# Kernel optimization log

Hardware: AMD Instinct MI355X
Metric: run time of the kernel (lower is better)

Reference implementation:

```python
import jax, jax.numpy as jnp
import numpy as np

N_NODES = 100000


def setup_inputs() -> dict:
    key = jax.random.key(0)
    k1, k2, k3, k4, k5 = jax.random.split(key, 5)
    dim_in, dim_out = 128, 128
    x = jax.random.normal(k1, (N_NODES, dim_in), dtype=jnp.float32)
    edge_index = jax.random.randint(k2, (2, 1600000), 0, N_NODES, dtype=jnp.int64)
    # PyG SAGEConv params: lin_l (neighbor path, with bias), lin_r (root path, no bias)
    s = 1.0 / np.sqrt(dim_in)
    W_l = jax.random.uniform(k3, (dim_in, dim_out), jnp.float32, -s, s)
    b_l = jax.random.uniform(k4, (dim_out,), jnp.float32, -s, s)
    W_r = jax.random.uniform(k5, (dim_in, dim_out), jnp.float32, -s, s)
    return {"x": x, "edge_index": edge_index, "W_l": W_l, "b_l": b_l, "W_r": W_r}


def reference(x, edge_index, W_l, b_l, W_r):
    src, dst = edge_index[0], edge_index[1]
    # mean aggregation of source features onto target nodes
    gathered = x[src]                                   # [E, d_in]
    summed = jax.ops.segment_sum(gathered, dst, num_segments=N_NODES)
    ones = jnp.ones((edge_index.shape[1],), dtype=x.dtype)
    count = jax.ops.segment_sum(ones, dst, num_segments=N_NODES)
    agg = summed / jnp.maximum(count, 1.0)[:, None]     # [N, d_in]
    # out = lin_l(agg) + lin_r(x)
    return agg @ W_l + b_l + x @ W_r
```

## Files before the change

kernel.cpp:

```cpp
#include <hip/hip_runtime.h>

#define N_NODES 100000
#define DIM 128
#define NE 1600000
#define NTILES (N_NODES / 8)
#define GEMM_BLOCKS 2048
#define CHUNK 512
#define NCHUNK ((N_NODES + CHUNK - 1) / CHUNK)

#define WT_BLOCKS 128
#define NCOARSE 391
#define CPAD 16
#define CCAP 4608
#define CB_BLOCKS 512
#define EPA (NE / CB_BLOCKS)
#define BCAP 640
#define NFINE 3125
#define BK_CAP 1024

typedef unsigned short u16;
typedef __attribute__((ext_vector_type(8))) short bf16x8;
typedef __attribute__((ext_vector_type(4))) float f32x4;

__device__ __forceinline__ float bf2f(u16 h) {
  return __uint_as_float(((unsigned int)h) << 16);
}
__device__ __forceinline__ u16 f2bf(float f) {
  unsigned int u = __float_as_uint(f);
  unsigned int lsb = (u >> 16) & 1u;
  u += 0x7fffu + lsb;
  return (u16)(u >> 16);
}


__global__ __launch_bounds__(256) void prep_k(const float* __restrict__ x,
                                              const float* __restrict__ Wl,
                                              const float* __restrict__ Wr,
                                              u16* __restrict__ Ax,
                                              u16* __restrict__ Wt,
                                              int* __restrict__ curC) {
  const int blk = blockIdx.x;
  if (blk < WT_BLOCKS) {
    int idx = blk * 256 + threadIdx.x;
    if (idx < NCOARSE * CPAD) curC[idx] = 0;
    int n = idx >> 8;
    int k = idx & 255;
    float v = (k < 128) ? Wr[(size_t)k * DIM + n] : Wl[(size_t)(k - 128) * DIM + n];
    Wt[(size_t)n * 256 + k] = f2bf(v);
    return;
  }
  int t = (blk - WT_BLOCKS) * 256 + threadIdx.x;
  int row = t >> 5;
  int c = (t & 31) * 4;
  float4 v = *(const float4*)(x + (size_t)row * DIM + c);
  ushort4 o;
  o.x = f2bf(v.x); o.y = f2bf(v.y); o.z = f2bf(v.z); o.w = f2bf(v.w);
  *(ushort4*)(Ax + (size_t)row * DIM + c) = o;
}

__global__ __launch_bounds__(512) void coarse_bin_k(const int* __restrict__ ei,
                                                    int* __restrict__ curC,
                                                    int* __restrict__ binnedC) {
  __shared__ u16 keyS[EPA];
  __shared__ int recS[EPA];
  __shared__ u16 key2[EPA];
  __shared__ int rec2[EPA];
  __shared__ int hist[NCOARSE];
  __shared__ int off[NCOARSE];
  __shared__ int lcur[NCOARSE];
  __shared__ int gbase[NCOARSE];
  __shared__ int scanb[512];
  const int tid = threadIdx.x;
  const int e0 = blockIdx.x * EPA;

  for (int i = tid; i < NCOARSE; i += 512) hist[i] = 0;
  __syncthreads();
  for (int i = tid; i < EPA; i += 512) {
    int src = ei[e0 + i];
    int dst = ei[NE + e0 + i];
    keyS[i] = (u16)(dst >> 8);
    recS[i] = ((dst & 255) << 17) | src;
    atomicAdd(&hist[dst >> 8], 1);
  }
  __syncthreads();
  int v = (tid < NCOARSE) ? hist[tid] : 0;
  scanb[tid] = v;
  __syncthreads();
  for (int o = 1; o < 512; o <<= 1) {
    int add = (tid >= o) ? scanb[tid - o] : 0;
    __syncthreads();
    scanb[tid] += add;
    __syncthreads();
  }
  if (tid < NCOARSE) {
    int ex = scanb[tid] - v;
    off[tid] = ex;
    lcur[tid] = ex;
    gbase[tid] = v ? atomicAdd(&curC[tid * CPAD], v) : 0;
  }
  __syncthreads();
  for (int i = tid; i < EPA; i += 512) {
    int k = keyS[i];
    int p = atomicAdd(&lcur[k], 1);
    rec2[p] = recS[i];
    key2[p] = (u16)k;
  }
  __syncthreads();
  for (int i = tid; i < EPA; i += 512) {
    int k = key2[i];
    int gp = gbase[k] + (i - off[k]);
    if (gp < CCAP) binnedC[(size_t)k * CCAP + gp] = rec2[i];
  }
}

__global__ __launch_bounds__(256) void fine_bin_k(const int* __restrict__ curC,
                                                  const int* __restrict__ binnedC,
                                                  int* __restrict__ binned,
                                                  int* __restrict__ bcnt) {
  __shared__ int recS[CCAP];
  __shared__ int rec2[CCAP];
  __shared__ int hist[8];
  __shared__ int off[8];
  __shared__ int lcur[8];
  const int c = blockIdx.x;
  const int tid = threadIdx.x;
  int cnt = curC[c * CPAD];
  if (cnt > CCAP) cnt = CCAP;

  if (tid < 8) hist[tid] = 0;
  __syncthreads();
  for (int i = tid; i < cnt; i += 256) {
    int r = binnedC[(size_t)c * CCAP + i];
    recS[i] = r;
    atomicAdd(&hist[r >> 22], 1);
  }
  __syncthreads();
  if (tid < 8) {
    int vv = hist[tid];
    bcnt[c * 8 + tid] = vv > BCAP ? BCAP : vv;
  }
  if (tid == 0) {
    int a = 0;
#pragma unroll
    for (int k = 0; k < 8; ++k) { off[k] = a; lcur[k] = a; a += hist[k]; }
  }
  __syncthreads();
  for (int i = tid; i < cnt; i += 256) {
    int r = recS[i];
    int p = atomicAdd(&lcur[r >> 22], 1);
    rec2[p] = r;
  }
  __syncthreads();
  for (int i = tid; i < cnt; i += 256) {
    int r = rec2[i];
    int k = r >> 22;
    int sl = i - off[k];
    if (sl < BCAP)
      binned[(size_t)(c * 8 + k) * BCAP + sl] = r & 0x3FFFFF;
  }
}

__global__ __launch_bounds__(256) void aggGemm_k(const int* __restrict__ bcnt,
                                                 const int* __restrict__ binned,
                                                 const u16* __restrict__ Ax,
                                                 const u16* __restrict__ Wt,
                                                 const float* __restrict__ bias,
                                                 float* __restrict__ out) {
  __shared__ int recS[BK_CAP];
  __shared__ int srcS[BK_CAP];
  __shared__ u16 aggS[32][136];
  __shared__ int hist[32];
  __shared__ int off[32];
  __shared__ int cur[32];
  const int b = blockIdx.x;
  const size_t lo = (size_t)b * BCAP;
  int cnt = bcnt[b];
  if (cnt > BK_CAP) cnt = BK_CAP;

  if (threadIdx.x < 32) hist[threadIdx.x] = 0;
  __syncthreads();
  for (int i = threadIdx.x; i < cnt; i += 256) {
    int rec = __builtin_nontemporal_load(&binned[lo + i]);
    recS[i] = rec;
    atomicAdd(&hist[rec >> 17], 1);
  }
  __syncthreads();
  if (threadIdx.x < 32) off[threadIdx.x] = hist[threadIdx.x];
  __syncthreads();
  for (int st = 1; st < 32; st <<= 1) {
    int add = 0;
    if (threadIdx.x < 32 && threadIdx.x >= st) add = off[threadIdx.x - st];
    __syncthreads();
    if (threadIdx.x < 32) off[threadIdx.x] += add;
    __syncthreads();
  }
  if (threadIdx.x < 32) cur[threadIdx.x] = off[threadIdx.x] - hist[threadIdx.x];
  __syncthreads();
  for (int i = threadIdx.x; i < cnt; i += 256) {
    int rec = recS[i];
    int l = atomicAdd(&cur[rec >> 17], 1);
    srcS[l] = (rec & 0x1FFFF) << 7;
  }
  __syncthreads();

  const int wave = threadIdx.x >> 6;
  const int lane = threadIdx.x & 63;
  const int half = lane >> 5;
  const int l5 = lane & 31;
  for (int ln = wave; ln < 32; ln += 4) {
    int d = hist[ln];
    int e1 = off[ln];
    int j = e1 - d;
    float a0 = 0.f, a1 = 0.f, a2 = 0.f, a3 = 0.f;
    for (; j + 4 <= e1; j += 4) {
      int sA = srcS[j + half];
      int sB = srcS[j + 2 + half];
      uint2 uA = *(const uint2*)(Ax + (size_t)(sA + l5 * 4));
      uint2 uB = *(const uint2*)(Ax + (size_t)(sB + l5 * 4));
      a0 += bf2f((u16)uA.x) + bf2f((u16)uB.x);
      a1 += bf2f((u16)(uA.x >> 16)) + bf2f((u16)(uB.x >> 16));
      a2 += bf2f((u16)uA.y) + bf2f((u16)uB.y);
      a3 += bf2f((u16)(uA.y >> 16)) + bf2f((u16)(uB.y >> 16));
    }
    if (j + 2 <= e1) {
      int sA = srcS[j + half];
      uint2 uA = *(const uint2*)(Ax + (size_t)(sA + l5 * 4));
      a0 += bf2f((u16)uA.x);
      a1 += bf2f((u16)(uA.x >> 16));
      a2 += bf2f((u16)uA.y);
      a3 += bf2f((u16)(uA.y >> 16));
      j += 2;
    }
    if (j < e1 && half == 0) {
      int sA = srcS[j];
      uint2 uA = *(const uint2*)(Ax + (size_t)(sA + l5 * 4));
      a0 += bf2f((u16)uA.x);
      a1 += bf2f((u16)(uA.x >> 16));
      a2 += bf2f((u16)uA.y);
      a3 += bf2f((u16)(uA.y >> 16));
    }
    a0 += __shfl_xor(a0, 32);
    a1 += __shfl_xor(a1, 32);
    a2 += __shfl_xor(a2, 32);
    a3 += __shfl_xor(a3, 32);
    if (half == 0) {
      float scale = 1.0f / fmaxf((float)d, 1.0f);
      uint2 pp;
      pp.x = (unsigned)f2bf(a0 * scale) | ((unsigned)f2bf(a1 * scale) << 16);
      pp.y = (unsigned)f2bf(a2 * scale) | ((unsigned)f2bf(a3 * scale) << 16);
      *(uint2*)&((unsigned*)aggS)[ln * 68 + l5 * 2] = pp;
    }
  }
  __syncthreads();

  const int m = lane & 15;
  const int q = lane >> 4;
  const int n0 = wave * 32;
  const float b0 = bias[n0 + m];
  const float b1 = bias[n0 + 16 + m];
  const u16* bp0 = Wt + (size_t)(n0 + m) * 256 + q * 8;
  const u16* bp1 = Wt + (size_t)(n0 + 16 + m) * 256 + q * 8;

#pragma clang loop unroll(disable)
  for (int t = 0; t < 2; ++t) {
    const int row = b * 32 + t * 16 + m;
    f32x4 acc0 = {0.f, 0.f, 0.f, 0.f};
    f32x4 acc1 = {0.f, 0.f, 0.f, 0.f};
    {
      const u16* apx = Ax + (size_t)row * DIM + q * 8;
      bf16x8 A0 = *(const bf16x8*)(apx + 0 * 32);
      bf16x8 A1 = *(const bf16x8*)(apx + 1 * 32);
      bf16x8 A2 = *(const bf16x8*)(apx + 2 * 32);
      bf16x8 A3 = *(const bf16x8*)(apx + 3 * 32);
      acc0 = __builtin_amdgcn_mfma_f32_16x16x32_bf16(A0, *(const bf16x8*)(bp0 + 0 * 32), acc0, 0, 0, 0);
      acc1 = __builtin_amdgcn_mfma_f32_16x16x32_bf16(A0, *(const bf16x8*)(bp1 + 0 * 32), acc1, 0, 0, 0);
      acc0 = __builtin_amdgcn_mfma_f32_16x16x32_bf16(A1, *(const bf16x8*)(bp0 + 1 * 32), acc0, 0, 0, 0);
      acc1 = __builtin_amdgcn_mfma_f32_16x16x32_bf16(A1, *(const bf16x8*)(bp1 + 1 * 32), acc1, 0, 0, 0);
      acc0 = __builtin_amdgcn_mfma_f32_16x16x32_bf16(A2, *(const bf16x8*)(bp0 + 2 * 32), acc0, 0, 0, 0);
      acc1 = __builtin_amdgcn_mfma_f32_16x16x32_bf16(A2, *(const bf16x8*)(bp1 + 2 * 32), acc1, 0, 0, 0);
      acc0 = __builtin_amdgcn_mfma_f32_16x16x32_bf16(A3, *(const bf16x8*)(bp0 + 3 * 32), acc0, 0, 0, 0);
      acc1 = __builtin_amdgcn_mfma_f32_16x16x32_bf16(A3, *(const bf16x8*)(bp1 + 3 * 32), acc1, 0, 0, 0);
    }
    {
      const u16* apg = &aggS[t * 16 + m][q * 8];
      bf16x8 A4 = *(const bf16x8*)(apg + 0 * 32);
      bf16x8 A5 = *(const bf16x8*)(apg + 1 * 32);
      bf16x8 A6 = *(const bf16x8*)(apg + 2 * 32);
      bf16x8 A7 = *(const bf16x8*)(apg + 3 * 32);
      acc0 = __builtin_amdgcn_mfma_f32_16x16x32_bf16(A4, *(const bf16x8*)(bp0 + 4 * 32), acc0, 0, 0, 0);
      acc1 = __builtin_amdgcn_mfma_f32_16x16x32_bf16(A4, *(const bf16x8*)(bp1 + 4 * 32), acc1, 0, 0, 0);
      acc0 = __builtin_amdgcn_mfma_f32_16x16x32_bf16(A5, *(const bf16x8*)(bp0 + 5 * 32), acc0, 0, 0, 0);
      acc1 = __builtin_amdgcn_mfma_f32_16x16x32_bf16(A5, *(const bf16x8*)(bp1 + 5 * 32), acc1, 0, 0, 0);
      acc0 = __builtin_amdgcn_mfma_f32_16x16x32_bf16(A6, *(const bf16x8*)(bp0 + 6 * 32), acc0, 0, 0, 0);
      acc1 = __builtin_amdgcn_mfma_f32_16x16x32_bf16(A6, *(const bf16x8*)(bp1 + 6 * 32), acc1, 0, 0, 0);
      acc0 = __builtin_amdgcn_mfma_f32_16x16x32_bf16(A7, *(const bf16x8*)(bp0 + 7 * 32), acc0, 0, 0, 0);
      acc1 = __builtin_amdgcn_mfma_f32_16x16x32_bf16(A7, *(const bf16x8*)(bp1 + 7 * 32), acc1, 0, 0, 0);
    }
    float* o = out + (size_t)(b * 32 + t * 16 + q * 4) * DIM + n0 + m;
#pragma unroll
    for (int r = 0; r < 4; ++r) {
      __builtin_nontemporal_store(acc0[r] + b0, &o[(size_t)r * DIM]);
      __builtin_nontemporal_store(acc1[r] + b1, &o[(size_t)r * DIM + 16]);
    }
  }
}

__global__ __launch_bounds__(256) void hist_k(const int* __restrict__ ei,
                                              int* __restrict__ deg) {
  int e = blockIdx.x * 256 + threadIdx.x;
  if (e < NE) atomicAdd(&deg[ei[NE + e]], 1);
}

__global__ __launch_bounds__(512) void scan_sum_k(const int* __restrict__ deg,
                                                  int* __restrict__ partials) {
  __shared__ int s[CHUNK];
  int i = blockIdx.x * CHUNK + threadIdx.x;
  s[threadIdx.x] = (i < N_NODES) ? deg[i] : 0;
  __syncthreads();
  for (int off = 256; off > 0; off >>= 1) {
    if (threadIdx.x < off) s[threadIdx.x] += s[threadIdx.x + off];
    __syncthreads();
  }
  if (threadIdx.x == 0) partials[blockIdx.x] = s[0];
}

__global__ __launch_bounds__(256) void scan_part_k(int* __restrict__ partials) {
  __shared__ int s[256];
  int t = threadIdx.x;
  int v = (t < NCHUNK) ? partials[t] : 0;
  s[t] = v;
  __syncthreads();
  for (int off = 1; off < 256; off <<= 1) {
    int add = (t >= off) ? s[t - off] : 0;
    __syncthreads();
    s[t] += add;
    __syncthreads();
  }
  if (t < NCHUNK) partials[t] = s[t] - v;
}

__global__ __launch_bounds__(512) void scan_out_k(const int* __restrict__ deg,
                                                  const int* __restrict__ partials,
                                                  int* __restrict__ offsets,
                                                  int* __restrict__ cursor) {
  __shared__ int s[CHUNK];
  int t = threadIdx.x;
  int i = blockIdx.x * CHUNK + t;
  int v = (i < N_NODES) ? deg[i] : 0;
  s[t] = v;
  __syncthreads();
  for (int off = 1; off < CHUNK; off <<= 1) {
    int add = (t >= off) ? s[t - off] : 0;
    __syncthreads();
    s[t] += add;
    __syncthreads();
  }
  if (i < N_NODES) {
    int excl = partials[blockIdx.x] + s[t] - v;
    offsets[i] = excl;
    cursor[i] = excl;
  }
  if (i == 0) offsets[N_NODES] = NE;
}

__global__ __launch_bounds__(256) void fill_k(const int* __restrict__ ei,
                                              int* __restrict__ cursor,
                                              int* __restrict__ csr) {
  int e = blockIdx.x * 256 + threadIdx.x;
  if (e < NE) {
    int dst = ei[NE + e];
    int pos = atomicAdd(&cursor[dst], 1);
    csr[pos] = ei[e];
  }
}

__global__ __launch_bounds__(256) void agg_f32_k(const int* __restrict__ offsets,
                                                 const int* __restrict__ csr,
                                                 const float* __restrict__ x,
                                                 float* __restrict__ agg) {
  int node = blockIdx.x * 4 + (threadIdx.x >> 6);
  int lane = threadIdx.x & 63;
  int beg = offsets[node], end = offsets[node + 1];
  float ax = 0.f, ay = 0.f;
  int i = beg;
  for (; i + 4 <= end; i += 4) {
    int s0 = csr[i], s1 = csr[i + 1], s2 = csr[i + 2], s3 = csr[i + 3];
    float2 v0 = *(const float2*)(x + (size_t)s0 * DIM + lane * 2);
    float2 v1 = *(const float2*)(x + (size_t)s1 * DIM + lane * 2);
    float2 v2 = *(const float2*)(x + (size_t)s2 * DIM + lane * 2);
    float2 v3 = *(const float2*)(x + (size_t)s3 * DIM + lane * 2);
    ax += v0.x + v1.x + v2.x + v3.x;
    ay += v0.y + v1.y + v2.y + v3.y;
  }
  for (; i < end; ++i) {
    float2 v0 = *(const float2*)(x + (size_t)csr[i] * DIM + lane * 2);
    ax += v0.x;
    ay += v0.y;
  }
  float scale = 1.0f / fmaxf((float)(end - beg), 1.0f);
  float2 r;
  r.x = ax * scale;
  r.y = ay * scale;
  *(float2*)(agg + (size_t)node * DIM + lane * 2) = r;
}

__global__ __launch_bounds__(256) void gemm_xw(const float* __restrict__ x,
                                               const float* __restrict__ W,
                                               const float* __restrict__ b,
                                               float* __restrict__ out) {
  __shared__ float Ws[DIM * DIM];
  for (int i = threadIdx.x; i < DIM * DIM; i += 256) Ws[i] = W[i];
  __syncthreads();
  const int c = threadIdx.x & 127;
  const int half = threadIdx.x >> 7;
  const float bias = b[c];
  for (int tile = blockIdx.x; tile < NTILES; tile += gridDim.x) {
    const int row0 = tile * 8 + half * 4;
    const float* r = x + (size_t)row0 * DIM;
    float a0 = 0.f, a1 = 0.f, a2 = 0.f, a3 = 0.f;
#pragma unroll 8
    for (int k4 = 0; k4 < 32; ++k4) {
      float4 p0 = *(const float4*)(r + 0 * DIM + k4 * 4);
      float4 p1 = *(const float4*)(r + 1 * DIM + k4 * 4);
      float4 p2 = *(const float4*)(r + 2 * DIM + k4 * 4);
      float4 p3 = *(const float4*)(r + 3 * DIM + k4 * 4);
      const float* wp = &Ws[k4 * 4 * DIM + c];
      float w0 = wp[0 * DIM], w1 = wp[1 * DIM], w2 = wp[2 * DIM], w3 = wp[3 * DIM];
      a0 += p0.x * w0 + p0.y * w1 + p0.z * w2 + p0.w * w3;
      a1 += p1.x * w0 + p1.y * w1 + p1.z * w2 + p1.w * w3;
      a2 += p2.x * w0 + p2.y * w1 + p2.z * w2 + p2.w * w3;
      a3 += p3.x * w0 + p3.y * w1 + p3.z * w2 + p3.w * w3;
    }
    out[(size_t)(row0 + 0) * DIM + c] = a0 + bias;
    out[(size_t)(row0 + 1) * DIM + c] = a1 + bias;
    out[(size_t)(row0 + 2) * DIM + c] = a2 + bias;
    out[(size_t)(row0 + 3) * DIM + c] = a3 + bias;
  }
}

__global__ __launch_bounds__(256) void gemm_aw(const float* __restrict__ agg,
                                               const float* __restrict__ W,
                                               float* __restrict__ out) {
  __shared__ float Ws[DIM * DIM];
  for (int i = threadIdx.x; i < DIM * DIM; i += 256) Ws[i] = W[i];
  __syncthreads();
  const int c = threadIdx.x & 127;
  const int half = threadIdx.x >> 7;
  for (int tile = blockIdx.x; tile < NTILES; tile += gridDim.x) {
    const int row0 = tile * 8 + half * 4;
    const float* r = agg + (size_t)row0 * DIM;
    float a0 = 0.f, a1 = 0.f, a2 = 0.f, a3 = 0.f;
#pragma unroll 8
    for (int k4 = 0; k4 < 32; ++k4) {
      float4 p0 = *(const float4*)(r + 0 * DIM + k4 * 4);
      float4 p1 = *(const float4*)(r + 1 * DIM + k4 * 4);
      float4 p2 = *(const float4*)(r + 2 * DIM + k4 * 4);
      float4 p3 = *(const float4*)(r + 3 * DIM + k4 * 4);
      const float* wp = &Ws[k4 * 4 * DIM + c];
      float w0 = wp[0 * DIM], w1 = wp[1 * DIM], w2 = wp[2 * DIM], w3 = wp[3 * DIM];
      a0 += p0.x * w0 + p0.y * w1 + p0.z * w2 + p0.w * w3;
      a1 += p1.x * w0 + p1.y * w1 + p1.z * w2 + p1.w * w3;
      a2 += p2.x * w0 + p2.y * w1 + p2.z * w2 + p2.w * w3;
      a3 += p3.x * w0 + p3.y * w1 + p3.z * w2 + p3.w * w3;
    }
    out[(size_t)(row0 + 0) * DIM + c] += a0;
    out[(size_t)(row0 + 1) * DIM + c] += a1;
    out[(size_t)(row0 + 2) * DIM + c] += a2;
    out[(size_t)(row0 + 3) * DIM + c] += a3;
  }
}

extern "C" void kernel_launch(void* const* d_in, const int* in_sizes, int n_in,
                              void* d_out, int out_size, void* d_ws, size_t ws_size,
                              hipStream_t stream) {
  const float* x  = (const float*)d_in[0];
  const int*   ei = (const int*)d_in[1];
  const float* Wl = (const float*)d_in[2];
  const float* bl = (const float*)d_in[3];
  const float* Wr = (const float*)d_in[4];
  float* out = (float*)d_out;

  u16* Ax       = (u16*)d_ws;
  u16* Ag       = Ax + (size_t)N_NODES * DIM;
  int* binnedC  = (int*)Ag;
  int* binned   = binnedC + (size_t)NCOARSE * CCAP;
  u16* Wt       = Ag + (size_t)N_NODES * DIM;
  int* curC     = (int*)(Wt + 128 * 256);
  int* bcnt     = curC + NCOARSE * CPAD;
  size_t needed = (size_t)N_NODES * DIM * 2 * 2 + 65536 +
                  (NCOARSE * CPAD + 3200) * 4;

  if (ws_size >= needed) {
    hipLaunchKernelGGL(prep_k, dim3(WT_BLOCKS + 12500), dim3(256), 0, stream,
                       x, Wl, Wr, Ax, Wt, curC);
    hipLaunchKernelGGL(coarse_bin_k, dim3(CB_BLOCKS), dim3(512), 0, stream,
                       ei, curC, binnedC);
    hipLaunchKernelGGL(fine_bin_k, dim3(NCOARSE), dim3(256), 0, stream,
                       curC, binnedC, binned, bcnt);
    hipLaunchKernelGGL(aggGemm_k, dim3(NFINE), dim3(256), 0, stream,
                       bcnt, binned, Ax, Wt, bl, out);
  } else {
    int* deg2      = (int*)d_ws;
    int* offsets2  = deg2 + N_NODES;
    int* partials2 = offsets2 + 100004;
    int* csr2      = partials2 + 256;
    float* agg     = (float*)(csr2 + NE);
    hipMemsetAsync(deg2, 0, (size_t)N_NODES * sizeof(int), stream);
    hipLaunchKernelGGL(hist_k, dim3((NE + 255) / 256), dim3(256), 0, stream, ei, deg2);
    hipLaunchKernelGGL(scan_sum_k, dim3(NCHUNK), dim3(CHUNK), 0, stream, deg2, partials2);
    hipLaunchKernelGGL(scan_part_k, dim3(1), dim3(256), 0, stream, partials2);
    hipLaunchKernelGGL(scan_out_k, dim3(NCHUNK), dim3(CHUNK), 0, stream,
                       deg2, partials2, offsets2, deg2);
    hipLaunchKernelGGL(fill_k, dim3((NE + 255) / 256), dim3(256), 0, stream,
                       ei, deg2, csr2);
    hipLaunchKernelGGL(agg_f32_k, dim3(N_NODES / 4), dim3(256), 0, stream,
                       offsets2, csr2, x, agg);
    hipLaunchKernelGGL(gemm_xw, dim3(GEMM_BLOCKS), dim3(256), 0, stream,
                       x, Wr, bl, out);
    hipLaunchKernelGGL(gemm_aw, dim3(GEMM_BLOCKS), dim3(256), 0, stream,
                       agg, Wl, out);
  }
}
```

Before: 236.8 us.

## Move per-node counting sort from aggGemm into fine_bin via 256-bucket histogram

fine_bin_k now sorts each coarse bin's edges by all 256 destination-node keys (prefix scan over 256 buckets) and writes per-node counts plus pre-shifted source offsets in final order. aggGemm_k then only reads the 32 per-node counts and copies the sorted source list into shared memory, with no histogram or local scatter of its own. This moves the fine-grained sort to 391 blocks instead of 3125 and shrinks aggGemm's shared memory. The cost is more shared memory and a longer scan in fine_bin_k, plus the clamping logic needed when a bin overflows BCAP.

```diff
diff --git a/kernel.cpp b/kernel.cpp
--- a/kernel.cpp
+++ b/kernel.cpp
@@ -16,7 +16,6 @@
 #define EPA (NE / CB_BLOCKS)
 #define BCAP 640
 #define NFINE 3125
-#define BK_CAP 1024
 
 typedef unsigned short u16;
 typedef __attribute__((ext_vector_type(8))) short bf16x8;
@@ -116,76 +115,79 @@
 __global__ __launch_bounds__(256) void fine_bin_k(const int* __restrict__ curC,
                                                   const int* __restrict__ binnedC,
                                                   int* __restrict__ binned,
-                                                  int* __restrict__ bcnt) {
+                                                  int* __restrict__ ncnt) {
   __shared__ int recS[CCAP];
   __shared__ int rec2[CCAP];
-  __shared__ int hist[8];
-  __shared__ int off[8];
-  __shared__ int lcur[8];
+  __shared__ u16 key2[CCAP];
+  __shared__ int hist[256];
+  __shared__ int off[256];
+  __shared__ int lcur[256];
+  __shared__ int foff[8];
   const int c = blockIdx.x;
   const int tid = threadIdx.x;
   int cnt = curC[c * CPAD];
   if (cnt > CCAP) cnt = CCAP;
 
-  if (tid < 8) hist[tid] = 0;
+  hist[tid] = 0;
   __syncthreads();
   for (int i = tid; i < cnt; i += 256) {
     int r = binnedC[(size_t)c * CCAP + i];
     recS[i] = r;
-    atomicAdd(&hist[r >> 22], 1);
-  }
-  __syncthreads();
-  if (tid < 8) {
-    int vv = hist[tid];
-    bcnt[c * 8 + tid] = vv > BCAP ? BCAP : vv;
-  }
-  if (tid == 0) {
-    int a = 0;
-#pragma unroll
-    for (int k = 0; k < 8; ++k) { off[k] = a; lcur[k] = a; a += hist[k]; }
-  }
+    atomicAdd(&hist[(r >> 17) & 255], 1);
+  }
+  __syncthreads();
+  int v = hist[tid];
+  ncnt[c * 256 + tid] = v;
+  off[tid] = v;
+  __syncthreads();
+  for (int o = 1; o < 256; o <<= 1) {
+    int add = (tid >= o) ? off[tid - o] : 0;
+    __syncthreads();
+    off[tid] += add;
+    __syncthreads();
+  }
+  int excl = off[tid] - v;
+  __syncthreads();
+  off[tid] = excl;
+  lcur[tid] = excl;
+  __syncthreads();
+  if (tid < 8) foff[tid] = off[tid * 32];
   __syncthreads();
   for (int i = tid; i < cnt; i += 256) {
     int r = recS[i];
-    int p = atomicAdd(&lcur[r >> 22], 1);
-    rec2[p] = r;
+    int p = atomicAdd(&lcur[(r >> 17) & 255], 1);
+    rec2[p] = (r & 0x1FFFF) << 7;
+    key2[p] = (u16)((r >> 17) & 255);
   }
   __syncthreads();
   for (int i = tid; i < cnt; i += 256) {
-    int r = rec2[i];
-    int k = r >> 22;
-    int sl = i - off[k];
+    int f = key2[i] >> 5;
+    int sl = i - foff[f];
     if (sl < BCAP)
-      binned[(size_t)(c * 8 + k) * BCAP + sl] = r & 0x3FFFFF;
-  }
-}
-
-__global__ __launch_bounds__(256) void aggGemm_k(const int* __restrict__ bcnt,
+      binned[(size_t)(c * 8 + f) * BCAP + sl] = rec2[i];
+  }
+}
+
+__global__ __launch_bounds__(256) void aggGemm_k(const int* __restrict__ ncnt,
                                                  const int* __restrict__ binned,
                                                  const u16* __restrict__ Ax,
                                                  const u16* __restrict__ Wt,
                                                  const float* __restrict__ bias,
                                                  float* __restrict__ out) {
-  __shared__ int recS[BK_CAP];
-  __shared__ int srcS[BK_CAP];
+  __shared__ int srcS[BCAP];
   __shared__ u16 aggS[32][136];
   __shared__ int hist[32];
   __shared__ int off[32];
-  __shared__ int cur[32];
+  __shared__ int cntS;
   const int b = blockIdx.x;
   const size_t lo = (size_t)b * BCAP;
-  int cnt = bcnt[b];
-  if (cnt > BK_CAP) cnt = BK_CAP;
-
-  if (threadIdx.x < 32) hist[threadIdx.x] = 0;
-  __syncthreads();
-  for (int i = threadIdx.x; i < cnt; i += 256) {
-    int rec = __builtin_nontemporal_load(&binned[lo + i]);
-    recS[i] = rec;
-    atomicAdd(&hist[rec >> 17], 1);
-  }
-  __syncthreads();
-  if (threadIdx.x < 32) off[threadIdx.x] = hist[threadIdx.x];
+  const int nbase = (b >> 3) * 256 + (b & 7) * 32;
+
+  if (threadIdx.x < 32) {
+    int d = ncnt[nbase + threadIdx.x];
+    hist[threadIdx.x] = d;
+    off[threadIdx.x] = d;
+  }
   __syncthreads();
   for (int st = 1; st < 32; st <<= 1) {
     int add = 0;
@@ -194,13 +196,11 @@
     if (threadIdx.x < 32) off[threadIdx.x] += add;
     __syncthreads();
   }
-  if (threadIdx.x < 32) cur[threadIdx.x] = off[threadIdx.x] - hist[threadIdx.x];
-  __syncthreads();
-  for (int i = threadIdx.x; i < cnt; i += 256) {
-    int rec = recS[i];
-    int l = atomicAdd(&cur[rec >> 17], 1);
-    srcS[l] = (rec & 0x1FFFF) << 7;
-  }
+  if (threadIdx.x == 0) cntS = off[31] > BCAP ? BCAP : off[31];
+  __syncthreads();
+  const int cnt = cntS;
+  for (int i = threadIdx.x; i < cnt; i += 256)
+    srcS[i] = __builtin_nontemporal_load(&binned[lo + i]);
   __syncthreads();
 
   const int wave = threadIdx.x >> 6;
@@ -210,7 +210,9 @@
   for (int ln = wave; ln < 32; ln += 4) {
     int d = hist[ln];
     int e1 = off[ln];
+    if (e1 > cnt) e1 = cnt;
     int j = e1 - d;
+    if (j < 0) j = 0;
     float a0 = 0.f, a1 = 0.f, a2 = 0.f, a3 = 0.f;
     for (; j + 4 <= e1; j += 4) {
       int sA = srcS[j + half];
@@ -486,9 +488,9 @@
   int* binned   = binnedC + (size_t)NCOARSE * CCAP;
   u16* Wt       = Ag + (size_t)N_NODES * DIM;
   int* curC     = (int*)(Wt + 128 * 256);
-  int* bcnt     = curC + NCOARSE * CPAD;
+  int* ncnt     = curC + NCOARSE * CPAD;
   size_t needed = (size_t)N_NODES * DIM * 2 * 2 + 65536 +
-                  (NCOARSE * CPAD + 3200) * 4;
+                  (NCOARSE * CPAD + NCOARSE * 256) * 4;
 
   if (ws_size >= needed) {
     hipLaunchKernelGGL(prep_k, dim3(WT_BLOCKS + 12500), dim3(256), 0, stream,
@@ -496,9 +498,9 @@
     hipLaunchKernelGGL(coarse_bin_k, dim3(CB_BLOCKS), dim3(512), 0, stream,
                        ei, curC, binnedC);
     hipLaunchKernelGGL(fine_bin_k, dim3(NCOARSE), dim3(256), 0, stream,
-                       curC, binnedC, binned, bcnt);
+                       curC, binnedC, binned, ncnt);
     hipLaunchKernelGGL(aggGemm_k, dim3(NFINE), dim3(256), 0, stream,
-                       bcnt, binned, Ax, Wt, bl, out);
+                       ncnt, binned, Ax, Wt, bl, out);
   } else {
     int* deg2      = (int*)d_ws;
     int* offsets2  = deg2 + N_NODES;
```

Result: no change. 237.6 us (+0.4%).
